# Optimization experiments

Measured on AMD Instinct MI355X. Metric: run time of the kernel, lower is better.

The kernel has to match this reference:

```python
import jax, jax.numpy as jnp
import numpy as np

N, E = 16384, 524288
IN_C, H1, H2 = 128, 128, 64
EDGE_F = 16
NB = 10                      # binary outputs
MC_GROUPS = (4, 6)           # multi-class group sizes (proto, service)
NC = 10                      # continuous outputs
EPS = 1e-5


def setup_inputs() -> dict:
    key = jax.random.key(0)
    ks = jax.random.split(key, 16)
    def lin(k, fan_in, fan_out):
        s = 1.0 / np.sqrt(fan_in)
        kw, kb = jax.random.split(k)
        return (jax.random.uniform(kw, (fan_in, fan_out), jnp.float32, -s, s),
                jax.random.uniform(kb, (fan_out,), jnp.float32, -s, s))
    w1, b1 = lin(ks[0], IN_C, H1)
    w2, b2 = lin(ks[1], H1, H2)
    w_bin, b_bin = lin(ks[2], H2, NB)
    w_mc, b_mc = lin(ks[3], H2, sum(MC_GROUPS))
    w_cont, b_cont = lin(ks[4], H2, NC)
    w_edge, b_edge = lin(ks[5], 2 * H2, EDGE_F)
    return {
        "x": jax.random.normal(ks[6], (N, IN_C), jnp.float32),
        "edge_index": jax.random.randint(ks[7], (2, E), 0, N, jnp.int64),
        "edge_attr": jax.random.normal(ks[8], (E, EDGE_F), jnp.float32),
        "w1": w1, "b1": b1,
        "bn1_g": jnp.ones((H1,), jnp.float32), "bn1_b": jnp.zeros((H1,), jnp.float32),
        "w2": w2, "b2": b2,
        "bn2_g": jnp.ones((H2,), jnp.float32), "bn2_b": jnp.zeros((H2,), jnp.float32),
        "w_bin": w_bin, "b_bin": b_bin,
        "w_mc": w_mc, "b_mc": b_mc,
        "w_cont": w_cont, "b_cont": b_cont,
        "w_edge": w_edge, "b_edge": b_edge,
    }


def _gcn(x, w, b, src, dst, norm, n):
    # GCNConv: x' = D^-1/2 (A+I) D^-1/2 (x W) + b
    h = x @ w
    msg = h[src] * norm[:, None]
    agg = jax.ops.segment_sum(msg, dst, num_segments=n)
    return agg + b


def _bn(h, g, b):
    m = jnp.mean(h, axis=0)
    v = jnp.var(h, axis=0)
    return g * (h - m) * jax.lax.rsqrt(v + EPS) + b


def reference(x, edge_index, edge_attr, w1, b1, bn1_g, bn1_b, w2, b2, bn2_g, bn2_b,
              w_bin, b_bin, w_mc, b_mc, w_cont, b_cont, w_edge, b_edge):
    n = x.shape[0]
    loops = jnp.arange(n, dtype=edge_index.dtype)
    src = jnp.concatenate([edge_index[0], loops])
    dst = jnp.concatenate([edge_index[1], loops])
    deg = jax.ops.segment_sum(jnp.ones_like(src, dtype=x.dtype), dst, num_segments=n)
    dis = jax.lax.rsqrt(deg)  # deg >= 1 thanks to self-loops
    norm = dis[src] * dis[dst]

    h = jax.nn.relu(_bn(_gcn(x, w1, b1, src, dst, norm, n), bn1_g, bn1_b))
    z = jax.nn.relu(_bn(_gcn(h, w2, b2, src, dst, norm, n), bn2_g, bn2_b))

    # node feature reconstruction: [binary sigmoid | per-group softmax | continuous]
    binary = jax.nn.sigmoid(z @ w_bin + b_bin)
    mc_logits = z @ w_mc + b_mc
    mc_parts, s = [], 0
    for g in MC_GROUPS:
        mc_parts.append(jax.nn.softmax(mc_logits[:, s:s + g], axis=1))
        s += g
    cont = z @ w_cont + b_cont
    reconstructed_x = jnp.concatenate([binary] + mc_parts + [cont], axis=1)

    adj = z @ z.T  # [N, N]

    edge_emb = jnp.concatenate([z[edge_index[0]], z[edge_index[1]]], axis=1)
    edge_features = edge_emb @ w_edge + b_edge
    return (reconstructed_x, adj, edge_features)
```

## Files before the change

kernel.cpp:

```cpp
#include <hip/hip_runtime.h>
#include <hip/hip_bf16.h>
#include <math.h>


constexpr int kN = 16384;
constexpr int kE = 524288;
constexpr float kEps = 1e-5f;

typedef __attribute__((ext_vector_type(8))) short short8v;
typedef __attribute__((ext_vector_type(4))) float f32x4;

__device__ inline float bf2f(short u) {
  return __uint_as_float(((unsigned)(unsigned short)u) << 16);
}

__global__ void zero_kernel(int* counts, float* sums1, float* sums2) {
  int i = blockIdx.x * 256 + threadIdx.x;
  if (i < kN) counts[i] = 0;
  if (i < 256) sums1[i] = 0.f;
  if (i < 128) sums2[i] = 0.f;
}

__global__ void hist_kernel(const int* __restrict__ dst, int* __restrict__ counts) {
  int e = blockIdx.x * 256 + threadIdx.x;
  if (e < kE) atomicAdd(&counts[dst[e]], 1);
}

__global__ __launch_bounds__(1024) void scan_kernel(const int* __restrict__ counts,
    int* __restrict__ offsets, int* __restrict__ pos, float* __restrict__ dis) {
  __shared__ int wave_tot[16];
  int tid = threadIdx.x;
  int base = tid * 16;
  int loc[16];
  int s = 0;
#pragma unroll
  for (int i = 0; i < 16; i++) { loc[i] = s; s += counts[base + i]; }
  int lane = tid & 63, wv = tid >> 6;
  int incl = s;
#pragma unroll
  for (int d = 1; d < 64; d <<= 1) {
    int v = __shfl_up(incl, d, 64);
    if (lane >= d) incl += v;
  }
  if (lane == 63) wave_tot[wv] = incl;
  __syncthreads();
  int woff = 0;
  for (int i = 0; i < wv; i++) woff += wave_tot[i];
  int excl = woff + incl - s;
#pragma unroll
  for (int i = 0; i < 16; i++) {
    int o = excl + loc[i];
    offsets[base + i] = o;
    pos[base + i] = o;
    dis[base + i] = rsqrtf((float)counts[base + i] + 1.0f);
  }
}

__global__ void fill_kernel(const int* __restrict__ src, const int* __restrict__ dst,
                            int* __restrict__ pos, int* __restrict__ csr_src) {
  int e = blockIdx.x * 256 + threadIdx.x;
  if (e < kE) {
    int d = dst[e];
    int p = atomicAdd(&pos[d], 1);
    csr_src[p] = src[e];
  }
}

template <int BC, bool AFFINE>
__global__ __launch_bounds__(256) void gemm_kernel(
    const float* __restrict__ A, const float* __restrict__ W,
    const float* __restrict__ scl, const float* __restrict__ shf,
    const float* __restrict__ dis, float* __restrict__ out) {
  constexpr int NJ = BC / 16;
  constexpr int WF4 = (32 * BC) / 4 / 256;
  __shared__ float xs[64 * 33];
  __shared__ float wsh[32 * BC];
  int tid = threadIdx.x;
  int tx = tid & 15, ty = tid >> 4;
  int r0 = blockIdx.x * 64;
  float acc[4][NJ];
#pragma unroll
  for (int r = 0; r < 4; r++)
#pragma unroll
    for (int j = 0; j < NJ; j++) acc[r][j] = 0.f;

  for (int kb = 0; kb < 128; kb += 32) {
    __syncthreads();
#pragma unroll
    for (int q = 0; q < 2; q++) {
      int f = tid + q * 256;
      int row = f >> 3, kq = f & 7;
      float4 v = *(const float4*)(A + (size_t)(r0 + row) * 128 + kb + kq * 4);
      if (AFFINE) {
        float4 s4 = *(const float4*)(scl + kb + kq * 4);
        float4 h4 = *(const float4*)(shf + kb + kq * 4);
        v.x = fmaxf(0.f, fmaf(v.x, s4.x, h4.x));
        v.y = fmaxf(0.f, fmaf(v.y, s4.y, h4.y));
        v.z = fmaxf(0.f, fmaf(v.z, s4.z, h4.z));
        v.w = fmaxf(0.f, fmaf(v.w, s4.w, h4.w));
      }
      int bb = row * 33 + kq * 4;
      xs[bb + 0] = v.x; xs[bb + 1] = v.y; xs[bb + 2] = v.z; xs[bb + 3] = v.w;
    }
#pragma unroll
    for (int q = 0; q < WF4; q++) {
      int f = tid + q * 256;
      int k = f / (BC / 4), cq = f % (BC / 4);
      *(float4*)&wsh[k * BC + cq * 4] =
          *(const float4*)(W + (size_t)(kb + k) * BC + cq * 4);
    }
    __syncthreads();
#pragma unroll
    for (int kk = 0; kk < 32; kk++) {
      float av[4];
#pragma unroll
      for (int r = 0; r < 4; r++) av[r] = xs[(ty * 4 + r) * 33 + kk];
#pragma unroll
      for (int j = 0; j < NJ; j++) {
        float bv = wsh[kk * BC + tx + j * 16];
#pragma unroll
        for (int r = 0; r < 4; r++) acc[r][j] = fmaf(av[r], bv, acc[r][j]);
      }
    }
  }
#pragma unroll
  for (int r = 0; r < 4; r++) {
    int row = r0 + ty * 4 + r;
    float dr = dis[row];
#pragma unroll
    for (int j = 0; j < NJ; j++)
      out[(size_t)row * BC + tx + j * 16] = acc[r][j] * dr;
  }
}

template <int C>
__global__ void agg_kernel(const float* __restrict__ hs, const int* __restrict__ csr_src,
                           const int* __restrict__ offsets, const int* __restrict__ counts,
                           const float* __restrict__ dis, float* __restrict__ t) {
  int d = blockIdx.x;
  int c = threadIdx.x;
  float acc = hs[(size_t)d * C + c];
  int s0 = offsets[d];
  int n = counts[d];
  int i = 0;
  for (; i + 4 <= n; i += 4) {
    int sa = csr_src[s0 + i];
    int sb = csr_src[s0 + i + 1];
    int sc = csr_src[s0 + i + 2];
    int sd = csr_src[s0 + i + 3];
    float va = hs[(size_t)sa * C + c];
    float vb = hs[(size_t)sb * C + c];
    float vc = hs[(size_t)sc * C + c];
    float vd = hs[(size_t)sd * C + c];
    acc += va; acc += vb; acc += vc; acc += vd;
  }
  for (; i < n; i++) acc += hs[(size_t)csr_src[s0 + i] * C + c];
  t[(size_t)d * C + c] = acc * dis[d];
}

template <int C>
__global__ __launch_bounds__(256) void stats_kernel(const float* __restrict__ t,
                                                    float* __restrict__ sums) {
  constexpr int RP = 256 / C;
  int c = threadIdx.x % C;
  int rr = threadIdx.x / C;
  float s = 0.f, s2 = 0.f;
  for (int r = blockIdx.x * RP + rr; r < kN; r += gridDim.x * RP) {
    float v = t[(size_t)r * C + c];
    s += v;
    s2 += v * v;
  }
  atomicAdd(&sums[c], s);
  atomicAdd(&sums[C + c], s2);
}

template <int C>
__global__ void finalize_kernel(const float* __restrict__ sums, const float* __restrict__ g,
                                const float* __restrict__ b, float* __restrict__ scale,
                                float* __restrict__ shift) {
  int c = threadIdx.x;
  float mean = sums[c] / (float)kN;
  float var = sums[C + c] / (float)kN - mean * mean;
  float inv = rsqrtf(var + kEps);
  float sc = g[c] * inv;
  scale[c] = sc;
  shift[c] = b[c] - mean * sc;
}

__global__ void applyz_kernel(const float* __restrict__ t2, const float* __restrict__ scale,
                              const float* __restrict__ shift, float* __restrict__ zf,
                              __hip_bfloat16* __restrict__ zb) {
  int i = blockIdx.x * 256 + threadIdx.x;
  int c = i & 63;
  float v = fmaxf(0.f, fmaf(t2[i], scale[c], shift[c]));
  zf[i] = v;
  zb[i] = __float2bfloat16(v);
}

__global__ __launch_bounds__(256) void heads_kernel(const float* __restrict__ zf,
    const float* __restrict__ wbin, const float* __restrict__ bbin,
    const float* __restrict__ wmc, const float* __restrict__ bmc,
    const float* __restrict__ wcont, const float* __restrict__ bcont,
    float* __restrict__ out0) {
  __shared__ float wT[30 * 64];
  __shared__ float bias[32];
  int tid = threadIdx.x;
  for (int idx = tid; idx < 1920; idx += 256) {
    int j = idx >> 6, k = idx & 63;
    const float* src = (j < 10) ? wbin : (j < 20) ? wmc : wcont;
    wT[idx] = src[k * 10 + (j % 10)];
  }
  if (tid < 30)
    bias[tid] = (tid < 10) ? bbin[tid] : (tid < 20) ? bmc[tid - 10] : bcont[tid - 20];
  __syncthreads();
  int n = blockIdx.x * 256 + tid;
  float zr[64];
  const float4* z4 = (const float4*)(zf + (size_t)n * 64);
#pragma unroll
  for (int q = 0; q < 16; q++) {
    float4 v = z4[q];
    zr[4 * q] = v.x; zr[4 * q + 1] = v.y; zr[4 * q + 2] = v.z; zr[4 * q + 3] = v.w;
  }
  float acc[30];
#pragma unroll
  for (int j = 0; j < 30; j++) {
    float s = bias[j];
#pragma unroll
    for (int kc = 0; kc < 16; kc++) {
      f32x4 wv = *(const f32x4*)&wT[j * 64 + kc * 4];
      s = fmaf(zr[4 * kc + 0], wv.x, s);
      s = fmaf(zr[4 * kc + 1], wv.y, s);
      s = fmaf(zr[4 * kc + 2], wv.z, s);
      s = fmaf(zr[4 * kc + 3], wv.w, s);
    }
    acc[j] = s;
  }
  float* o = out0 + (size_t)n * 30;
#pragma unroll
  for (int j = 0; j < 10; j++) o[j] = 1.f / (1.f + expf(-acc[j]));
  float m1 = fmaxf(fmaxf(acc[10], acc[11]), fmaxf(acc[12], acc[13]));
  float e1[4], s1 = 0.f;
#pragma unroll
  for (int j = 0; j < 4; j++) { e1[j] = expf(acc[10 + j] - m1); s1 += e1[j]; }
#pragma unroll
  for (int j = 0; j < 4; j++) o[10 + j] = e1[j] / s1;
  float m2 = acc[14];
#pragma unroll
  for (int j = 15; j < 20; j++) m2 = fmaxf(m2, acc[j]);
  float e2[6], s2 = 0.f;
#pragma unroll
  for (int j = 0; j < 6; j++) { e2[j] = expf(acc[14 + j] - m2); s2 += e2[j]; }
#pragma unroll
  for (int j = 0; j < 6; j++) o[14 + j] = e2[j] / s2;
#pragma unroll
  for (int j = 0; j < 10; j++) o[20 + j] = acc[20 + j];
}

__global__ __launch_bounds__(256) void adj_kernel(const short* __restrict__ zb,
                                                  float* __restrict__ adj) {
  __shared__ float cs[128 * 132];
  int tid = threadIdx.x;
  int wid = tid >> 6, lane = tid & 63;
  int li0 = (wid >> 1) * 64;
  int lj0 = (wid & 1) * 64;
  int i0 = blockIdx.x * 128 + li0;
  int j0 = blockIdx.y * 128 + lj0;
  int lr = lane & 15, lg = lane >> 4;
  short8v a[4][2], b[4][2];
#pragma unroll
  for (int mt = 0; mt < 4; mt++)
#pragma unroll
    for (int ks = 0; ks < 2; ks++)
      a[mt][ks] = *(const short8v*)(zb + (size_t)(i0 + mt * 16 + lr) * 64 + ks * 32 + lg * 8);
#pragma unroll
  for (int nt = 0; nt < 4; nt++)
#pragma unroll
    for (int ks = 0; ks < 2; ks++)
      b[nt][ks] = *(const short8v*)(zb + (size_t)(j0 + nt * 16 + lr) * 64 + ks * 32 + lg * 8);
  f32x4 acc[4][4];
#pragma unroll
  for (int mt = 0; mt < 4; mt++)
#pragma unroll
    for (int nt = 0; nt < 4; nt++) {
      f32x4 zz = {0.f, 0.f, 0.f, 0.f};
      acc[mt][nt] = zz;
    }
#pragma unroll
  for (int ks = 0; ks < 2; ks++)
#pragma unroll
    for (int mt = 0; mt < 4; mt++)
#pragma unroll
      for (int nt = 0; nt < 4; nt++)
        acc[mt][nt] = __builtin_amdgcn_mfma_f32_16x16x32_bf16(a[mt][ks], b[nt][ks],
                                                              acc[mt][nt], 0, 0, 0);
#pragma unroll
  for (int mt = 0; mt < 4; mt++)
#pragma unroll
    for (int nt = 0; nt < 4; nt++)
#pragma unroll
      for (int r = 0; r < 4; r++)
        cs[(li0 + mt * 16 + lg * 4 + r) * 132 + lj0 + nt * 16 + lr] = acc[mt][nt][r];
  __syncthreads();
  int row = tid >> 5;
  int c4 = tid & 31;
  size_t gbase = (size_t)(blockIdx.x * 128 + row) * kN + blockIdx.y * 128 + c4 * 4;
  const float* lbase = &cs[row * 132 + c4 * 4];
#pragma unroll
  for (int it = 0; it < 16; it++) {
    f32x4 v = *(const f32x4*)(lbase + it * 8 * 132);
    *(f32x4*)(adj + gbase + (size_t)it * 8 * kN) = v;
  }
}

__global__ __launch_bounds__(256) void edge_kernel(const short* __restrict__ zb,
    const int* __restrict__ srcs, const int* __restrict__ dsts,
    const float* __restrict__ we, const float* __restrict__ be,
    float* __restrict__ eout) {
  __shared__ float w[2048];
  __shared__ float bb[16];
  int tid = threadIdx.x;
  for (int i = tid; i < 2048; i += 256) w[i] = we[i];
  if (tid < 16) bb[tid] = be[tid];
  __syncthreads();
  int base = blockIdx.x * 1024 + tid;
  int s[4], d[4];
#pragma unroll
  for (int i = 0; i < 4; i++) { s[i] = srcs[base + i * 256]; d[i] = dsts[base + i * 256]; }
  float acc[4][16];
#pragma unroll
  for (int i = 0; i < 4; i++)
#pragma unroll
    for (int f = 0; f < 16; f++) acc[i][f] = bb[f];

#pragma unroll 2
  for (int q = 0; q < 8; q++) {
    short8v v[4];
#pragma unroll
    for (int i = 0; i < 4; i++)
      v[i] = *(const short8v*)(zb + (size_t)s[i] * 64 + q * 8);
#pragma unroll
    for (int t = 0; t < 8; t++) {
      float vt[4];
#pragma unroll
      for (int i = 0; i < 4; i++) vt[i] = bf2f(v[i][t]);
#pragma unroll
      for (int fc = 0; fc < 4; fc++) {
        f32x4 wv = *(const f32x4*)&w[(q * 8 + t) * 16 + fc * 4];
#pragma unroll
        for (int i = 0; i < 4; i++) {
          acc[i][fc * 4 + 0] = fmaf(vt[i], wv.x, acc[i][fc * 4 + 0]);
          acc[i][fc * 4 + 1] = fmaf(vt[i], wv.y, acc[i][fc * 4 + 1]);
          acc[i][fc * 4 + 2] = fmaf(vt[i], wv.z, acc[i][fc * 4 + 2]);
          acc[i][fc * 4 + 3] = fmaf(vt[i], wv.w, acc[i][fc * 4 + 3]);
        }
      }
    }
  }
#pragma unroll 2
  for (int q = 0; q < 8; q++) {
    short8v v[4];
#pragma unroll
    for (int i = 0; i < 4; i++)
      v[i] = *(const short8v*)(zb + (size_t)d[i] * 64 + q * 8);
#pragma unroll
    for (int t = 0; t < 8; t++) {
      float vt[4];
#pragma unroll
      for (int i = 0; i < 4; i++) vt[i] = bf2f(v[i][t]);
#pragma unroll
      for (int fc = 0; fc < 4; fc++) {
        f32x4 wv = *(const f32x4*)&w[1024 + (q * 8 + t) * 16 + fc * 4];
#pragma unroll
        for (int i = 0; i < 4; i++) {
          acc[i][fc * 4 + 0] = fmaf(vt[i], wv.x, acc[i][fc * 4 + 0]);
          acc[i][fc * 4 + 1] = fmaf(vt[i], wv.y, acc[i][fc * 4 + 1]);
          acc[i][fc * 4 + 2] = fmaf(vt[i], wv.z, acc[i][fc * 4 + 2]);
          acc[i][fc * 4 + 3] = fmaf(vt[i], wv.w, acc[i][fc * 4 + 3]);
        }
      }
    }
  }
#pragma unroll
  for (int i = 0; i < 4; i++) {
    float4* o4 = (float4*)(eout + (size_t)(base + i * 256) * 16);
    o4[0] = make_float4(acc[i][0], acc[i][1], acc[i][2], acc[i][3]);
    o4[1] = make_float4(acc[i][4], acc[i][5], acc[i][6], acc[i][7]);
    o4[2] = make_float4(acc[i][8], acc[i][9], acc[i][10], acc[i][11]);
    o4[3] = make_float4(acc[i][12], acc[i][13], acc[i][14], acc[i][15]);
  }
}

extern "C" void kernel_launch(void* const* d_in, const int* in_sizes, int n_in,
                              void* d_out, int out_size, void* d_ws, size_t ws_size,
                              hipStream_t stream) {
  const float* x      = (const float*)d_in[0];
  const int*   ei     = (const int*)d_in[1];
  const float* w1     = (const float*)d_in[3];
  const float* bn1_g  = (const float*)d_in[5];
  const float* bn1_b  = (const float*)d_in[6];
  const float* w2     = (const float*)d_in[7];
  const float* bn2_g  = (const float*)d_in[9];
  const float* bn2_b  = (const float*)d_in[10];
  const float* w_bin  = (const float*)d_in[11];
  const float* b_bin  = (const float*)d_in[12];
  const float* w_mc   = (const float*)d_in[13];
  const float* b_mc   = (const float*)d_in[14];
  const float* w_cont = (const float*)d_in[15];
  const float* b_cont = (const float*)d_in[16];
  const float* w_edge = (const float*)d_in[17];
  const float* b_edge = (const float*)d_in[18];

  float* out0 = (float*)d_out;
  float* adj  = out0 + (size_t)kN * 30;
  float* eout = adj + (size_t)kN * kN;

  char* wp = (char*)d_ws;
  auto alloc = [&](size_t bytes) {
    char* p = wp;
    wp += (bytes + 255) & ~(size_t)255;
    return p;
  };
  int*   counts  = (int*)alloc((size_t)kN * 4);
  int*   offsets = (int*)alloc((size_t)kN * 4);
  int*   pos     = (int*)alloc((size_t)kN * 4);
  int*   csr_src = (int*)alloc((size_t)kE * 4);
  float* dis     = (float*)alloc((size_t)kN * 4);
  float* sums1   = (float*)alloc(256 * 4);
  float* sums2   = (float*)alloc(128 * 4);
  float* scale1  = (float*)alloc(128 * 4);
  float* shift1  = (float*)alloc(128 * 4);
  float* scale2  = (float*)alloc(64 * 4);
  float* shift2  = (float*)alloc(64 * 4);
  float* hs1     = (float*)alloc((size_t)kN * 128 * 4);
  float* t1      = (float*)alloc((size_t)kN * 128 * 4);
  float* hs2     = (float*)alloc((size_t)kN * 64 * 4);
  float* t2      = (float*)alloc((size_t)kN * 64 * 4);
  float* zf      = (float*)alloc((size_t)kN * 64 * 4);
  __hip_bfloat16* zb = (__hip_bfloat16*)alloc((size_t)kN * 64 * 2);

  const int* esrc = ei;
  const int* edst = ei + kE;

  zero_kernel<<<dim3(64), dim3(256), 0, stream>>>(counts, sums1, sums2);
  hist_kernel<<<dim3(2048), dim3(256), 0, stream>>>(edst, counts);
  scan_kernel<<<dim3(1), dim3(1024), 0, stream>>>(counts, offsets, pos, dis);
  fill_kernel<<<dim3(2048), dim3(256), 0, stream>>>(esrc, edst, pos, csr_src);

  gemm_kernel<128, false><<<dim3(kN / 64), dim3(256), 0, stream>>>(
      x, w1, nullptr, nullptr, dis, hs1);
  agg_kernel<128><<<dim3(kN), dim3(128), 0, stream>>>(hs1, csr_src, offsets, counts, dis, t1);
  stats_kernel<128><<<dim3(256), dim3(256), 0, stream>>>(t1, sums1);
  finalize_kernel<128><<<dim3(1), dim3(128), 0, stream>>>(sums1, bn1_g, bn1_b, scale1, shift1);

  gemm_kernel<64, true><<<dim3(kN / 64), dim3(256), 0, stream>>>(
      t1, w2, scale1, shift1, dis, hs2);
  agg_kernel<64><<<dim3(kN), dim3(64), 0, stream>>>(hs2, csr_src, offsets, counts, dis, t2);
  stats_kernel<64><<<dim3(256), dim3(256), 0, stream>>>(t2, sums2);
  finalize_kernel<64><<<dim3(1), dim3(64), 0, stream>>>(sums2, bn2_g, bn2_b, scale2, shift2);

  applyz_kernel<<<dim3(kN * 64 / 256), dim3(256), 0, stream>>>(t2, scale2, shift2, zf, zb);

  heads_kernel<<<dim3(kN / 256), dim3(256), 0, stream>>>(
      zf, w_bin, b_bin, w_mc, b_mc, w_cont, b_cont, out0);
  adj_kernel<<<dim3(kN / 128, kN / 128), dim3(256), 0, stream>>>((const short*)zb, adj);
  edge_kernel<<<dim3(kE / 1024), dim3(256), 0, stream>>>((const short*)zb, esrc, edst,
                                                         w_edge, b_edge, eout);
}
```

Before: 480.7 us.

## Store GCN intermediates in bf16, fold BN finalize, use MFMA edge kernel

Intermediate GCN buffers (hs1, t1, hs2) are now stored as bf16, roughly halving the gather and stats traffic in the aggregation kernels. The BatchNorm finalize step is folded into the next consumer kernels (gemm2, applyz), removing two tiny launches. The edge-feature projection moves from scalar FMAs to bf16 MFMA, with the edge weights pre-swizzled into fragment layout inside zero_kernel. This trades some precision in the intermediate features for less bandwidth and fewer launches. The adjacency GEMM, which writes the 1 GB output, still dominates the total time.

```diff
diff --git a/kernel.cpp b/kernel.cpp
--- a/kernel.cpp
+++ b/kernel.cpp
@@ -10,15 +10,22 @@
 typedef __attribute__((ext_vector_type(8))) short short8v;
 typedef __attribute__((ext_vector_type(4))) float f32x4;
 
-__device__ inline float bf2f(short u) {
-  return __uint_as_float(((unsigned)(unsigned short)u) << 16);
-}
-
-__global__ void zero_kernel(int* counts, float* sums1, float* sums2) {
+__device__ inline float bf2f(unsigned short u) {
+  return __uint_as_float(((unsigned)u) << 16);
+}
+
+__global__ void zero_kernel(int* counts, float* sums1, float* sums2,
+                            const float* __restrict__ we, __hip_bfloat16* wfr) {
   int i = blockIdx.x * 256 + threadIdx.x;
   if (i < kN) counts[i] = 0;
   if (i < 256) sums1[i] = 0.f;
   if (i < 128) sums2[i] = 0.f;
+  if (i < 2048) {
+    int f = i >> 9, l = (i >> 3) & 63, j = i & 7;
+    int lr = l & 15, lg = l >> 4;
+    int krow = f * 32 + lg * 8 + j;
+    wfr[i] = __float2bfloat16(we[krow * 16 + lr]);
+  }
 }
 
 __global__ void hist_kernel(const int* __restrict__ dst, int* __restrict__ counts) {
@@ -66,13 +73,10 @@
   }
 }
 
-template <int BC, bool AFFINE>
-__global__ __launch_bounds__(256) void gemm_kernel(
+__global__ __launch_bounds__(256) void gemm1_kernel(
     const float* __restrict__ A, const float* __restrict__ W,
-    const float* __restrict__ scl, const float* __restrict__ shf,
-    const float* __restrict__ dis, float* __restrict__ out) {
-  constexpr int NJ = BC / 16;
-  constexpr int WF4 = (32 * BC) / 4 / 256;
+    const float* __restrict__ dis, __hip_bfloat16* __restrict__ out) {
+  constexpr int BC = 128, NJ = 8, WF4 = 4;
   __shared__ float xs[64 * 33];
   __shared__ float wsh[32 * BC];
   int tid = threadIdx.x;
@@ -91,14 +95,6 @@
       int f = tid + q * 256;
       int row = f >> 3, kq = f & 7;
       float4 v = *(const float4*)(A + (size_t)(r0 + row) * 128 + kb + kq * 4);
-      if (AFFINE) {
-        float4 s4 = *(const float4*)(scl + kb + kq * 4);
-        float4 h4 = *(const float4*)(shf + kb + kq * 4);
-        v.x = fmaxf(0.f, fmaf(v.x, s4.x, h4.x));
-        v.y = fmaxf(0.f, fmaf(v.y, s4.y, h4.y));
-        v.z = fmaxf(0.f, fmaf(v.z, s4.z, h4.z));
-        v.w = fmaxf(0.f, fmaf(v.w, s4.w, h4.w));
-      }
       int bb = row * 33 + kq * 4;
       xs[bb + 0] = v.x; xs[bb + 1] = v.y; xs[bb + 2] = v.z; xs[bb + 3] = v.w;
     }
@@ -129,17 +125,88 @@
     float dr = dis[row];
 #pragma unroll
     for (int j = 0; j < NJ; j++)
-      out[(size_t)row * BC + tx + j * 16] = acc[r][j] * dr;
-  }
-}
-
-template <int C>
-__global__ void agg_kernel(const float* __restrict__ hs, const int* __restrict__ csr_src,
-                           const int* __restrict__ offsets, const int* __restrict__ counts,
-                           const float* __restrict__ dis, float* __restrict__ t) {
+      out[(size_t)row * BC + tx + j * 16] = __float2bfloat16(acc[r][j] * dr);
+  }
+}
+
+__global__ __launch_bounds__(256) void gemm2_kernel(
+    const unsigned short* __restrict__ A, const float* __restrict__ W,
+    const float* __restrict__ sums, const float* __restrict__ g,
+    const float* __restrict__ b, const float* __restrict__ dis,
+    __hip_bfloat16* __restrict__ out) {
+  constexpr int BC = 64, NJ = 4, WF4 = 2;
+  __shared__ float xs[64 * 33];
+  __shared__ float wsh[32 * BC];
+  __shared__ float s_scl[128], s_shf[128];
+  int tid = threadIdx.x;
+  if (tid < 128) {
+    float mean = sums[tid] / (float)kN;
+    float var = sums[128 + tid] / (float)kN - mean * mean;
+    float inv = rsqrtf(var + kEps);
+    float sc = g[tid] * inv;
+    s_scl[tid] = sc;
+    s_shf[tid] = b[tid] - mean * sc;
+  }
+  int tx = tid & 15, ty = tid >> 4;
+  int r0 = blockIdx.x * 64;
+  float acc[4][NJ];
+#pragma unroll
+  for (int r = 0; r < 4; r++)
+#pragma unroll
+    for (int j = 0; j < NJ; j++) acc[r][j] = 0.f;
+
+  for (int kb = 0; kb < 128; kb += 32) {
+    __syncthreads();
+    {
+      int row = tid >> 2, kq = tid & 3;
+      short8v v8 = *(const short8v*)(A + (size_t)(r0 + row) * 128 + kb + kq * 8);
+      int bb = row * 33 + kq * 8;
+#pragma unroll
+      for (int j = 0; j < 8; j++) {
+        int c = kb + kq * 8 + j;
+        float v = bf2f((unsigned short)v8[j]);
+        xs[bb + j] = fmaxf(0.f, fmaf(v, s_scl[c], s_shf[c]));
+      }
+    }
+#pragma unroll
+    for (int q = 0; q < WF4; q++) {
+      int f = tid + q * 256;
+      int k = f / (BC / 4), cq = f % (BC / 4);
+      *(float4*)&wsh[k * BC + cq * 4] =
+          *(const float4*)(W + (size_t)(kb + k) * BC + cq * 4);
+    }
+    __syncthreads();
+#pragma unroll
+    for (int kk = 0; kk < 32; kk++) {
+      float av[4];
+#pragma unroll
+      for (int r = 0; r < 4; r++) av[r] = xs[(ty * 4 + r) * 33 + kk];
+#pragma unroll
+      for (int j = 0; j < NJ; j++) {
+        float bv = wsh[kk * BC + tx + j * 16];
+#pragma unroll
+        for (int r = 0; r < 4; r++) acc[r][j] = fmaf(av[r], bv, acc[r][j]);
+      }
+    }
+  }
+#pragma unroll
+  for (int r = 0; r < 4; r++) {
+    int row = r0 + ty * 4 + r;
+    float dr = dis[row];
+#pragma unroll
+    for (int j = 0; j < NJ; j++)
+      out[(size_t)row * BC + tx + j * 16] = __float2bfloat16(acc[r][j] * dr);
+  }
+}
+
+template <int C, bool OBF16>
+__global__ void agg_kernel(const unsigned short* __restrict__ hs,
+                           const int* __restrict__ csr_src, const int* __restrict__ offsets,
+                           const int* __restrict__ counts, const float* __restrict__ dis,
+                           void* __restrict__ tout) {
   int d = blockIdx.x;
   int c = threadIdx.x;
-  float acc = hs[(size_t)d * C + c];
+  float acc = bf2f(hs[(size_t)d * C + c]);
   int s0 = offsets[d];
   int n = counts[d];
   int i = 0;
@@ -148,25 +215,31 @@
     int sb = csr_src[s0 + i + 1];
     int sc = csr_src[s0 + i + 2];
     int sd = csr_src[s0 + i + 3];
-    float va = hs[(size_t)sa * C + c];
-    float vb = hs[(size_t)sb * C + c];
-    float vc = hs[(size_t)sc * C + c];
-    float vd = hs[(size_t)sd * C + c];
+    float va = bf2f(hs[(size_t)sa * C + c]);
+    float vb = bf2f(hs[(size_t)sb * C + c]);
+    float vc = bf2f(hs[(size_t)sc * C + c]);
+    float vd = bf2f(hs[(size_t)sd * C + c]);
     acc += va; acc += vb; acc += vc; acc += vd;
   }
-  for (; i < n; i++) acc += hs[(size_t)csr_src[s0 + i] * C + c];
-  t[(size_t)d * C + c] = acc * dis[d];
-}
-
-template <int C>
-__global__ __launch_bounds__(256) void stats_kernel(const float* __restrict__ t,
+  for (; i < n; i++) acc += bf2f(hs[(size_t)csr_src[s0 + i] * C + c]);
+  float r = acc * dis[d];
+  if constexpr (OBF16)
+    ((__hip_bfloat16*)tout)[(size_t)d * C + c] = __float2bfloat16(r);
+  else
+    ((float*)tout)[(size_t)d * C + c] = r;
+}
+
+template <int C, bool BF16>
+__global__ __launch_bounds__(256) void stats_kernel(const void* __restrict__ t,
                                                     float* __restrict__ sums) {
   constexpr int RP = 256 / C;
   int c = threadIdx.x % C;
   int rr = threadIdx.x / C;
   float s = 0.f, s2 = 0.f;
   for (int r = blockIdx.x * RP + rr; r < kN; r += gridDim.x * RP) {
-    float v = t[(size_t)r * C + c];
+    float v;
+    if constexpr (BF16) v = bf2f(((const unsigned short*)t)[(size_t)r * C + c]);
+    else v = ((const float*)t)[(size_t)r * C + c];
     s += v;
     s2 += v * v;
   }
@@ -174,25 +247,24 @@
   atomicAdd(&sums[C + c], s2);
 }
 
-template <int C>
-__global__ void finalize_kernel(const float* __restrict__ sums, const float* __restrict__ g,
-                                const float* __restrict__ b, float* __restrict__ scale,
-                                float* __restrict__ shift) {
-  int c = threadIdx.x;
-  float mean = sums[c] / (float)kN;
-  float var = sums[C + c] / (float)kN - mean * mean;
-  float inv = rsqrtf(var + kEps);
-  float sc = g[c] * inv;
-  scale[c] = sc;
-  shift[c] = b[c] - mean * sc;
-}
-
-__global__ void applyz_kernel(const float* __restrict__ t2, const float* __restrict__ scale,
-                              const float* __restrict__ shift, float* __restrict__ zf,
-                              __hip_bfloat16* __restrict__ zb) {
-  int i = blockIdx.x * 256 + threadIdx.x;
+__global__ __launch_bounds__(256) void applyz_kernel(const float* __restrict__ t2,
+    const float* __restrict__ sums, const float* __restrict__ g,
+    const float* __restrict__ b, float* __restrict__ zf,
+    __hip_bfloat16* __restrict__ zb) {
+  __shared__ float s_scl[64], s_shf[64];
+  int tid = threadIdx.x;
+  if (tid < 64) {
+    float mean = sums[tid] / (float)kN;
+    float var = sums[64 + tid] / (float)kN - mean * mean;
+    float inv = rsqrtf(var + kEps);
+    float sc = g[tid] * inv;
+    s_scl[tid] = sc;
+    s_shf[tid] = b[tid] - mean * sc;
+  }
+  __syncthreads();
+  int i = blockIdx.x * 256 + tid;
   int c = i & 63;
-  float v = fmaxf(0.f, fmaf(t2[i], scale[c], shift[c]));
+  float v = fmaxf(0.f, fmaf(t2[i], s_scl[c], s_shf[c]));
   zf[i] = v;
   zb[i] = __float2bfloat16(v);
 }
@@ -312,81 +384,34 @@
   }
 }
 
-__global__ __launch_bounds__(256) void edge_kernel(const short* __restrict__ zb,
+__global__ __launch_bounds__(256) void edge_mfma_kernel(const short* __restrict__ zb,
     const int* __restrict__ srcs, const int* __restrict__ dsts,
-    const float* __restrict__ we, const float* __restrict__ be,
+    const short* __restrict__ wfr, const float* __restrict__ be,
     float* __restrict__ eout) {
-  __shared__ float w[2048];
-  __shared__ float bb[16];
-  int tid = threadIdx.x;
-  for (int i = tid; i < 2048; i += 256) w[i] = we[i];
-  if (tid < 16) bb[tid] = be[tid];
-  __syncthreads();
-  int base = blockIdx.x * 1024 + tid;
-  int s[4], d[4];
-#pragma unroll
-  for (int i = 0; i < 4; i++) { s[i] = srcs[base + i * 256]; d[i] = dsts[base + i * 256]; }
-  float acc[4][16];
-#pragma unroll
-  for (int i = 0; i < 4; i++)
-#pragma unroll
-    for (int f = 0; f < 16; f++) acc[i][f] = bb[f];
-
-#pragma unroll 2
-  for (int q = 0; q < 8; q++) {
-    short8v v[4];
-#pragma unroll
-    for (int i = 0; i < 4; i++)
-      v[i] = *(const short8v*)(zb + (size_t)s[i] * 64 + q * 8);
-#pragma unroll
-    for (int t = 0; t < 8; t++) {
-      float vt[4];
-#pragma unroll
-      for (int i = 0; i < 4; i++) vt[i] = bf2f(v[i][t]);
-#pragma unroll
-      for (int fc = 0; fc < 4; fc++) {
-        f32x4 wv = *(const f32x4*)&w[(q * 8 + t) * 16 + fc * 4];
-#pragma unroll
-        for (int i = 0; i < 4; i++) {
-          acc[i][fc * 4 + 0] = fmaf(vt[i], wv.x, acc[i][fc * 4 + 0]);
-          acc[i][fc * 4 + 1] = fmaf(vt[i], wv.y, acc[i][fc * 4 + 1]);
-          acc[i][fc * 4 + 2] = fmaf(vt[i], wv.z, acc[i][fc * 4 + 2]);
-          acc[i][fc * 4 + 3] = fmaf(vt[i], wv.w, acc[i][fc * 4 + 3]);
-        }
-      }
-    }
-  }
-#pragma unroll 2
-  for (int q = 0; q < 8; q++) {
-    short8v v[4];
-#pragma unroll
-    for (int i = 0; i < 4; i++)
-      v[i] = *(const short8v*)(zb + (size_t)d[i] * 64 + q * 8);
-#pragma unroll
-    for (int t = 0; t < 8; t++) {
-      float vt[4];
-#pragma unroll
-      for (int i = 0; i < 4; i++) vt[i] = bf2f(v[i][t]);
-#pragma unroll
-      for (int fc = 0; fc < 4; fc++) {
-        f32x4 wv = *(const f32x4*)&w[1024 + (q * 8 + t) * 16 + fc * 4];
-#pragma unroll
-        for (int i = 0; i < 4; i++) {
-          acc[i][fc * 4 + 0] = fmaf(vt[i], wv.x, acc[i][fc * 4 + 0]);
-          acc[i][fc * 4 + 1] = fmaf(vt[i], wv.y, acc[i][fc * 4 + 1]);
-          acc[i][fc * 4 + 2] = fmaf(vt[i], wv.z, acc[i][fc * 4 + 2]);
-          acc[i][fc * 4 + 3] = fmaf(vt[i], wv.w, acc[i][fc * 4 + 3]);
-        }
-      }
-    }
-  }
-#pragma unroll
-  for (int i = 0; i < 4; i++) {
-    float4* o4 = (float4*)(eout + (size_t)(base + i * 256) * 16);
-    o4[0] = make_float4(acc[i][0], acc[i][1], acc[i][2], acc[i][3]);
-    o4[1] = make_float4(acc[i][4], acc[i][5], acc[i][6], acc[i][7]);
-    o4[2] = make_float4(acc[i][8], acc[i][9], acc[i][10], acc[i][11]);
-    o4[3] = make_float4(acc[i][12], acc[i][13], acc[i][14], acc[i][15]);
+  int tid = threadIdx.x;
+  int wv = tid >> 6, lane = tid & 63;
+  int gw = blockIdx.x * 4 + wv;
+  int lr = lane & 15, lg = lane >> 4;
+  short8v bfr[4];
+#pragma unroll
+  for (int f = 0; f < 4; f++)
+    bfr[f] = *(const short8v*)(wfr + ((size_t)f * 64 + lane) * 8);
+  float bias = be[lr];
+  for (int t = 0; t < 8; t++) {
+    int e0 = (gw * 8 + t) * 16;
+    int se = srcs[e0 + lr], de = dsts[e0 + lr];
+    short8v a0 = *(const short8v*)(zb + (size_t)se * 64 + lg * 8);
+    short8v a1 = *(const short8v*)(zb + (size_t)se * 64 + 32 + lg * 8);
+    short8v a2 = *(const short8v*)(zb + (size_t)de * 64 + lg * 8);
+    short8v a3 = *(const short8v*)(zb + (size_t)de * 64 + 32 + lg * 8);
+    f32x4 acc = {0.f, 0.f, 0.f, 0.f};
+    acc = __builtin_amdgcn_mfma_f32_16x16x32_bf16(a0, bfr[0], acc, 0, 0, 0);
+    acc = __builtin_amdgcn_mfma_f32_16x16x32_bf16(a1, bfr[1], acc, 0, 0, 0);
+    acc = __builtin_amdgcn_mfma_f32_16x16x32_bf16(a2, bfr[2], acc, 0, 0, 0);
+    acc = __builtin_amdgcn_mfma_f32_16x16x32_bf16(a3, bfr[3], acc, 0, 0, 0);
+#pragma unroll
+    for (int r = 0; r < 4; r++)
+      eout[(size_t)(e0 + lg * 4 + r) * 16 + lr] = acc[r] + bias;
   }
 }
 
@@ -427,42 +452,39 @@
   float* dis     = (float*)alloc((size_t)kN * 4);
   float* sums1   = (float*)alloc(256 * 4);
   float* sums2   = (float*)alloc(128 * 4);
-  float* scale1  = (float*)alloc(128 * 4);
-  float* shift1  = (float*)alloc(128 * 4);
-  float* scale2  = (float*)alloc(64 * 4);
-  float* shift2  = (float*)alloc(64 * 4);
-  float* hs1     = (float*)alloc((size_t)kN * 128 * 4);
-  float* t1      = (float*)alloc((size_t)kN * 128 * 4);
-  float* hs2     = (float*)alloc((size_t)kN * 64 * 4);
+  __hip_bfloat16* hs1 = (__hip_bfloat16*)alloc((size_t)kN * 128 * 2);
+  __hip_bfloat16* t1  = (__hip_bfloat16*)alloc((size_t)kN * 128 * 2);
+  __hip_bfloat16* hs2 = (__hip_bfloat16*)alloc((size_t)kN * 64 * 2);
   float* t2      = (float*)alloc((size_t)kN * 64 * 4);
   float* zf      = (float*)alloc((size_t)kN * 64 * 4);
-  __hip_bfloat16* zb = (__hip_bfloat16*)alloc((size_t)kN * 64 * 2);
+  __hip_bfloat16* zb  = (__hip_bfloat16*)alloc((size_t)kN * 64 * 2);
+  __hip_bfloat16* wfr = (__hip_bfloat16*)alloc(2048 * 2);
 
   const int* esrc = ei;
   const int* edst = ei + kE;
 
-  zero_kernel<<<dim3(64), dim3(256), 0, stream>>>(counts, sums1, sums2);
+  zero_kernel<<<dim3(64), dim3(256), 0, stream>>>(counts, sums1, sums2, w_edge, wfr);
   hist_kernel<<<dim3(2048), dim3(256), 0, stream>>>(edst, counts);
   scan_kernel<<<dim3(1), dim3(1024), 0, stream>>>(counts, offsets, pos, dis);
   fill_kernel<<<dim3(2048), dim3(256), 0, stream>>>(esrc, edst, pos, csr_src);
 
-  gemm_kernel<128, false><<<dim3(kN / 64), dim3(256), 0, stream>>>(
-      x, w1, nullptr, nullptr, dis, hs1);
-  agg_kernel<128><<<dim3(kN), dim3(128), 0, stream>>>(hs1, csr_src, offsets, counts, dis, t1);
-  stats_kernel<128><<<dim3(256), dim3(256), 0, stream>>>(t1, sums1);
-  finalize_kernel<128><<<dim3(1), dim3(128), 0, stream>>>(sums1, bn1_g, bn1_b, scale1, shift1);
-
-  gemm_kernel<64, true><<<dim3(kN / 64), dim3(256), 0, stream>>>(
-      t1, w2, scale1, shift1, dis, hs2);
-  agg_kernel<64><<<dim3(kN), dim3(64), 0, stream>>>(hs2, csr_src, offsets, counts, dis, t2);
-  stats_kernel<64><<<dim3(256), dim3(256), 0, stream>>>(t2, sums2);
-  finalize_kernel<64><<<dim3(1), dim3(64), 0, stream>>>(sums2, bn2_g, bn2_b, scale2, shift2);
-
-  applyz_kernel<<<dim3(kN * 64 / 256), dim3(256), 0, stream>>>(t2, scale2, shift2, zf, zb);
+  gemm1_kernel<<<dim3(kN / 64), dim3(256), 0, stream>>>(x, w1, dis, hs1);
+  agg_kernel<128, true><<<dim3(kN), dim3(128), 0, stream>>>(
+      (const unsigned short*)hs1, csr_src, offsets, counts, dis, t1);
+  stats_kernel<128, true><<<dim3(256), dim3(256), 0, stream>>>(t1, sums1);
+
+  gemm2_kernel<<<dim3(kN / 64), dim3(256), 0, stream>>>(
+      (const unsigned short*)t1, w2, sums1, bn1_g, bn1_b, dis, hs2);
+  agg_kernel<64, false><<<dim3(kN), dim3(64), 0, stream>>>(
+      (const unsigned short*)hs2, csr_src, offsets, counts, dis, t2);
+  stats_kernel<64, false><<<dim3(256), dim3(256), 0, stream>>>(t2, sums2);
+
+  applyz_kernel<<<dim3(kN * 64 / 256), dim3(256), 0, stream>>>(
+      t2, sums2, bn2_g, bn2_b, zf, zb);
 
   heads_kernel<<<dim3(kN / 256), dim3(256), 0, stream>>>(
       zf, w_bin, b_bin, w_mc, b_mc, w_cont, b_cont, out0);
   adj_kernel<<<dim3(kN / 128, kN / 128), dim3(256), 0, stream>>>((const short*)zb, adj);
-  edge_kernel<<<dim3(kE / 1024), dim3(256), 0, stream>>>((const short*)zb, esrc, edst,
-                                                         w_edge, b_edge, eout);
-}
+  edge_mfma_kernel<<<dim3(1024), dim3(256), 0, stream>>>(
+      (const short*)zb, esrc, edst, (const short*)wfr, b_edge, eout);
+}
```

Measured after the change: 442.2 us. 1.09x faster.
